# Kernel tuning notes

Measured on AMD Instinct MI355X. Metric: run time of the kernel, lower is better.

## Reference

```python
import jax, jax.numpy as jnp
import numpy as np

N_NODES = 50000
N_EDGES = 800000
F_IN = 16
F_EDGE = 8
H = 8  # latent_dim = [8, 8]
NUM_GRAPHS = 512


def setup_inputs() -> dict:
    key = jax.random.key(0)
    ks = jax.random.split(key, 16)
    x = jax.random.normal(ks[0], (N_NODES, F_IN), dtype=jnp.float32)
    edge_index = jax.random.randint(ks[1], (2, N_EDGES), 0, N_NODES)
    edge_attr = jax.random.normal(ks[2], (N_EDGES, F_EDGE), dtype=jnp.float32)
    batch = jnp.sort(jax.random.randint(ks[3], (N_NODES,), 0, NUM_GRAPHS))
    s = 0.1
    # edge MLPs (single Linear each): edge_attr -> flattened [in, out] weight
    We1 = jax.random.normal(ks[4], (F_EDGE, F_IN * H), dtype=jnp.float32) * s
    be1 = jnp.zeros((F_IN * H,), dtype=jnp.float32)
    We2 = jax.random.normal(ks[5], (F_EDGE, H * H), dtype=jnp.float32) * s
    be2 = jnp.zeros((H * H,), dtype=jnp.float32)
    # NNConv root weights + biases
    root1 = jax.random.normal(ks[6], (F_IN, H), dtype=jnp.float32) * s
    b1 = jnp.zeros((H,), dtype=jnp.float32)
    root2 = jax.random.normal(ks[7], (H, H), dtype=jnp.float32) * s
    b2 = jnp.zeros((H,), dtype=jnp.float32)
    # final readout linear H -> 1
    Wlast = jax.random.normal(ks[8], (H, 1), dtype=jnp.float32) * s
    blast = jnp.zeros((1,), dtype=jnp.float32)
    return {"x": x, "edge_index": edge_index, "edge_attr": edge_attr, "batch": batch,
            "We1": We1, "be1": be1, "root1": root1, "b1": b1,
            "We2": We2, "be2": be2, "root2": root2, "b2": b2,
            "Wlast": Wlast, "blast": blast}


def _nnconv(x, src, dst, edge_attr, We, be, root, b, in_dim, out_dim):
    # per-edge weight matrix from edge MLP: [E, in_dim, out_dim]
    W = (edge_attr @ We + be).reshape(-1, in_dim, out_dim)
    # gather source features, per-edge matvec, scatter-add to targets
    msg = jnp.einsum('ei,eio->eo', x[src], W)            # [E, out_dim]
    agg = jax.ops.segment_sum(msg, dst, num_segments=x.shape[0])
    return agg + x @ root + b                            # root weight + bias


def reference(x, edge_index, edge_attr, batch, We1, be1, root1, b1,
              We2, be2, root2, b2, Wlast, blast):
    src, dst = edge_index[0], edge_index[1]
    h = jax.nn.relu(_nnconv(x, src, dst, edge_attr, We1, be1, root1, b1, F_IN, H))
    h = jax.nn.relu(_nnconv(h, src, dst, edge_attr, We2, be2, root2, b2, H, H))
    # per-graph sum pooling (vectorized equivalent of the python loop)
    pooled = jax.ops.segment_sum(h, batch, num_segments=NUM_GRAPHS)  # [G, H]
    return pooled @ Wlast + blast                                    # [G, 1]
```

## Files before the change

kernel.cpp:

```cpp
#include <hip/hip_runtime.h>

#define F_EDGE 8
#define H 8

__device__ __forceinline__ unsigned short f2bf(float f) {
    unsigned u = __float_as_uint(f);
    unsigned r = u + 0x7fffu + ((u >> 16) & 1u);
    return (unsigned short)(r >> 16);
}
__device__ __forceinline__ float bflo(unsigned u) { return __uint_as_float(u << 16); }
__device__ __forceinline__ float bfhi(unsigned u) { return __uint_as_float(u & 0xffff0000u); }

__global__ __launch_bounds__(256) void pack_kernel(
    const int* __restrict__ ei, const float* __restrict__ ea,
    int2* __restrict__ sd, unsigned short* __restrict__ eab, int E) {
    int e = blockIdx.x * 256 + threadIdx.x;
    if (e >= E) return;
    sd[e] = make_int2(ei[e], ei[E + e]);
    const float4* av = (const float4*)(ea + (long long)e * F_EDGE);
    float4 a0 = av[0], a1 = av[1];
    uint4 pw;
    pw.x = (unsigned)f2bf(a0.x) | ((unsigned)f2bf(a0.y) << 16);
    pw.y = (unsigned)f2bf(a0.z) | ((unsigned)f2bf(a0.w) << 16);
    pw.z = (unsigned)f2bf(a1.x) | ((unsigned)f2bf(a1.y) << 16);
    pw.w = (unsigned)f2bf(a1.z) | ((unsigned)f2bf(a1.w) << 16);
    *(uint4*)(eab + (long long)e * F_EDGE) = pw;
}

template <int IN, bool RELU, bool INIT>
__global__ __launch_bounds__(256) void prep_kernel(
    const float* __restrict__ feat, const float* __restrict__ We,
    const float* __restrict__ be, const float* __restrict__ root,
    const float* __restrict__ b, unsigned short* __restrict__ Pt,
    float* __restrict__ q, float* __restrict__ aggseed, int n_nodes,
    float* __restrict__ out, const float* __restrict__ blast, int out_n) {
    __shared__ float sW[IN * H * 12];
    int tid = threadIdx.x;
    for (int t = tid; t < IN * H * 12; t += 256) {
        int r = t / 12, m = t - r * 12;
        float v = 0.f;
        if (m < 8) v = We[m * (IN * H) + r];
        else if (m == 8) v = be[r];
        else if (m == 9) v = root[r];
        sW[t] = v;
    }
    if (INIT && blockIdx.x == 0) {
        float bl = blast[0];
        for (int t = tid; t < out_n; t += 256) out[t] = bl;
    }
    __syncthreads();

    int n = blockIdx.x * 32 + (tid >> 3);
    if (n >= n_nodes) return;
    int j = tid & 7;

    float f[IN];
    const float4* fv = (const float4*)(feat + (long long)n * IN);
#pragma unroll
    for (int i4 = 0; i4 < IN / 4; ++i4) {
        float4 v = fv[i4];
        f[i4 * 4 + 0] = v.x; f[i4 * 4 + 1] = v.y;
        f[i4 * 4 + 2] = v.z; f[i4 * 4 + 3] = v.w;
    }
    if (RELU) {
#pragma unroll
        for (int i = 0; i < IN; ++i) f[i] = f[i] > 0.f ? f[i] : 0.f;
    }

    float p[8] = {0.f, 0.f, 0.f, 0.f, 0.f, 0.f, 0.f, 0.f};
    float qq = 0.f, hr = 0.f;
#pragma unroll
    for (int i = 0; i < IN; ++i) {
        const float* row = &sW[(i * 8 + j) * 12];
        float4 w0 = *(const float4*)row;
        float4 w1 = *(const float4*)(row + 4);
        float2 br = *(const float2*)(row + 8);
        float fi = f[i];
        p[0] = fmaf(fi, w0.x, p[0]); p[1] = fmaf(fi, w0.y, p[1]);
        p[2] = fmaf(fi, w0.z, p[2]); p[3] = fmaf(fi, w0.w, p[3]);
        p[4] = fmaf(fi, w1.x, p[4]); p[5] = fmaf(fi, w1.y, p[5]);
        p[6] = fmaf(fi, w1.z, p[6]); p[7] = fmaf(fi, w1.w, p[7]);
        qq = fmaf(fi, br.x, qq);
        hr = fmaf(fi, br.y, hr);
    }
    uint4 pw;
    pw.x = (unsigned)f2bf(p[0]) | ((unsigned)f2bf(p[1]) << 16);
    pw.y = (unsigned)f2bf(p[2]) | ((unsigned)f2bf(p[3]) << 16);
    pw.z = (unsigned)f2bf(p[4]) | ((unsigned)f2bf(p[5]) << 16);
    pw.w = (unsigned)f2bf(p[6]) | ((unsigned)f2bf(p[7]) << 16);
    *(uint4*)(Pt + ((long long)n * H + j) * F_EDGE) = pw;
    q[(long long)n * H + j] = qq;
    aggseed[(long long)n * H + j] = hr + b[j];
}

__global__ __launch_bounds__(256) void edge_fact_kernel(
    const int2* __restrict__ sd, const unsigned short* __restrict__ eab,
    const unsigned short* __restrict__ Pt, const float* __restrict__ q,
    float* __restrict__ agg, int E) {
    long long gid = (long long)blockIdx.x * 256 + threadIdx.x;
    int e = (int)(gid >> 3);
    if (e >= E) return;
    int j = (int)(gid & 7);

    int2 se = sd[e];
    uint4 av = *(const uint4*)(eab + (long long)e * F_EDGE);
    uint4 pw = *(const uint4*)(Pt + ((long long)se.x * H + j) * F_EDGE);
    float m = q[(long long)se.x * H + j];

    m = fmaf(bflo(av.x), bflo(pw.x), m);
    m = fmaf(bfhi(av.x), bfhi(pw.x), m);
    m = fmaf(bflo(av.y), bflo(pw.y), m);
    m = fmaf(bfhi(av.y), bfhi(pw.y), m);
    m = fmaf(bflo(av.z), bflo(pw.z), m);
    m = fmaf(bfhi(av.z), bfhi(pw.z), m);
    m = fmaf(bflo(av.w), bflo(pw.w), m);
    m = fmaf(bfhi(av.w), bfhi(pw.w), m);

    unsafeAtomicAdd(&agg[(long long)se.y * H + j], m);
}

__global__ __launch_bounds__(256) void pool_kernel(
    const float* __restrict__ h2pre, const int* __restrict__ batch,
    const float* __restrict__ Wlast, float* __restrict__ out,
    int n_nodes, int n_graphs) {
    __shared__ float bins[512];
    bool use_bins = (n_graphs <= 512);
    if (use_bins) {
        for (int t = threadIdx.x; t < n_graphs; t += 256) bins[t] = 0.f;
        __syncthreads();
    }
    float wl[8];
#pragma unroll
    for (int j = 0; j < 8; ++j) wl[j] = Wlast[j];

    int base = blockIdx.x * 1024;
#pragma unroll
    for (int r = 0; r < 4; ++r) {
        int n = base + r * 256 + threadIdx.x;
        if (n < n_nodes) {
            const float4* hv = (const float4*)(h2pre + (long long)n * H);
            float4 h0 = hv[0], h1 = hv[1];
            float c = 0.f;
            c = fmaf(fmaxf(h0.x, 0.f), wl[0], c);
            c = fmaf(fmaxf(h0.y, 0.f), wl[1], c);
            c = fmaf(fmaxf(h0.z, 0.f), wl[2], c);
            c = fmaf(fmaxf(h0.w, 0.f), wl[3], c);
            c = fmaf(fmaxf(h1.x, 0.f), wl[4], c);
            c = fmaf(fmaxf(h1.y, 0.f), wl[5], c);
            c = fmaf(fmaxf(h1.z, 0.f), wl[6], c);
            c = fmaf(fmaxf(h1.w, 0.f), wl[7], c);
            if (use_bins) atomicAdd(&bins[batch[n]], c);
            else unsafeAtomicAdd(&out[batch[n]], c);
        }
    }
    if (use_bins) {
        __syncthreads();
        for (int t = threadIdx.x; t < n_graphs; t += 256) {
            float v = bins[t];
            if (v != 0.f) unsafeAtomicAdd(&out[t], v);
        }
    }
}

extern "C" void kernel_launch(void* const* d_in, const int* in_sizes, int n_in,
                              void* d_out, int out_size, void* d_ws, size_t ws_size,
                              hipStream_t stream) {
    const float* x     = (const float*)d_in[0];
    const int*   ei    = (const int*)d_in[1];
    const float* ea    = (const float*)d_in[2];
    const int*   batch = (const int*)d_in[3];
    const float* We1   = (const float*)d_in[4];
    const float* be1   = (const float*)d_in[5];
    const float* root1 = (const float*)d_in[6];
    const float* b1    = (const float*)d_in[7];
    const float* We2   = (const float*)d_in[8];
    const float* be2   = (const float*)d_in[9];
    const float* root2 = (const float*)d_in[10];
    const float* b2    = (const float*)d_in[11];
    const float* Wlast = (const float*)d_in[12];
    const float* blast = (const float*)d_in[13];
    float* out = (float*)d_out;

    int F_IN_rt = 16;
    int n_nodes = in_sizes[0] / F_IN_rt;
    int E = in_sizes[1] / 2;

    char* w = (char*)d_ws;
    auto take = [&](size_t bytes) {
        char* p = w;
        w += (bytes + 15) & ~(size_t)15;
        return p;
    };
    unsigned short* Pt1 = (unsigned short*)take((size_t)n_nodes * H * F_EDGE * 2);
    unsigned short* Pt2 = (unsigned short*)take((size_t)n_nodes * H * F_EDGE * 2);
    float* q1    = (float*)take((size_t)n_nodes * H * 4);
    float* q2    = (float*)take((size_t)n_nodes * H * 4);
    float* h1    = (float*)take((size_t)n_nodes * H * 4);
    float* h2    = (float*)take((size_t)n_nodes * H * 4);
    int2* sd     = (int2*)take((size_t)E * 8);
    unsigned short* eab = (unsigned short*)take((size_t)E * F_EDGE * 2);

    int nbe = (E + 255) / 256;

    pack_kernel<<<nbe, 256, 0, stream>>>(ei, ea, sd, eab, E);

    int nblocks = (n_nodes + 31) / 32;
    prep_kernel<16, false, true><<<nblocks, 256, 0, stream>>>(
        x, We1, be1, root1, b1, Pt1, q1, h1, n_nodes, out, blast, out_size);

    long long lanes = (long long)E * H;
    int eblks = (int)((lanes + 255) / 256);
    edge_fact_kernel<<<eblks, 256, 0, stream>>>(sd, eab, Pt1, q1, h1, E);

    prep_kernel<H, true, false><<<nblocks, 256, 0, stream>>>(
        h1, We2, be2, root2, b2, Pt2, q2, h2, n_nodes, nullptr, nullptr, 0);

    edge_fact_kernel<<<eblks, 256, 0, stream>>>(sd, eab, Pt2, q2, h2, E);

    int pblocks = (n_nodes + 1023) / 1024;
    pool_kernel<<<pblocks, 256, 0, stream>>>(h2, batch, Wlast, out, n_nodes, out_size);
}
```

Measured before the change: 204.3 us.

## Fuse all phases into one cooperative persistent kernel with grid syncs

Replaces the six separate launches with one cooperative mega-kernel that runs prep, edge, prep, edge and pool phases, separated by grid-wide barriers and using grid-stride loops. The pack kernel is removed, so edges read the int indices and fp32 edge attributes directly instead of a packed bf16 copy. This aims to cut launch gaps and the extra pass over the edges. In exchange the edge phase reads more bytes per edge, occupancy is capped at a persistent grid, and four grid syncs are added. The old multi-launch path is kept as a fallback if the cooperative launch fails.

Measured after the change: 459.7 us. +125.0%, slower.

```diff
diff --git a/kernel.cpp b/kernel.cpp
--- a/kernel.cpp
+++ b/kernel.cpp
@@ -1,4 +1,7 @@
 #include <hip/hip_runtime.h>
+#include <hip/hip_cooperative_groups.h>
+
+namespace cg = cooperative_groups;
 
 #define F_EDGE 8
 #define H 8
@@ -11,30 +14,14 @@
 __device__ __forceinline__ float bflo(unsigned u) { return __uint_as_float(u << 16); }
 __device__ __forceinline__ float bfhi(unsigned u) { return __uint_as_float(u & 0xffff0000u); }
 
-__global__ __launch_bounds__(256) void pack_kernel(
-    const int* __restrict__ ei, const float* __restrict__ ea,
-    int2* __restrict__ sd, unsigned short* __restrict__ eab, int E) {
-    int e = blockIdx.x * 256 + threadIdx.x;
-    if (e >= E) return;
-    sd[e] = make_int2(ei[e], ei[E + e]);
-    const float4* av = (const float4*)(ea + (long long)e * F_EDGE);
-    float4 a0 = av[0], a1 = av[1];
-    uint4 pw;
-    pw.x = (unsigned)f2bf(a0.x) | ((unsigned)f2bf(a0.y) << 16);
-    pw.y = (unsigned)f2bf(a0.z) | ((unsigned)f2bf(a0.w) << 16);
-    pw.z = (unsigned)f2bf(a1.x) | ((unsigned)f2bf(a1.y) << 16);
-    pw.w = (unsigned)f2bf(a1.z) | ((unsigned)f2bf(a1.w) << 16);
-    *(uint4*)(eab + (long long)e * F_EDGE) = pw;
-}
-
-template <int IN, bool RELU, bool INIT>
-__global__ __launch_bounds__(256) void prep_kernel(
+
+template <int IN, bool RELU>
+__device__ __forceinline__ void prep_phase(
     const float* __restrict__ feat, const float* __restrict__ We,
     const float* __restrict__ be, const float* __restrict__ root,
     const float* __restrict__ b, unsigned short* __restrict__ Pt,
     float* __restrict__ q, float* __restrict__ aggseed, int n_nodes,
-    float* __restrict__ out, const float* __restrict__ blast, int out_n) {
-    __shared__ float sW[IN * H * 12];
+    float* smem) {
     int tid = threadIdx.x;
     for (int t = tid; t < IN * H * 12; t += 256) {
         int r = t / 12, m = t - r * 12;
@@ -42,124 +29,192 @@
         if (m < 8) v = We[m * (IN * H) + r];
         else if (m == 8) v = be[r];
         else if (m == 9) v = root[r];
-        sW[t] = v;
-    }
+        smem[t] = v;
+    }
+    __syncthreads();
+
+    int U = (n_nodes + 31) >> 5;
+    int j = tid & 7;
+    for (int u = blockIdx.x; u < U; u += gridDim.x) {
+        int n = u * 32 + (tid >> 3);
+        if (n >= n_nodes) continue;
+
+        float f[IN];
+        const float4* fv = (const float4*)(feat + (long long)n * IN);
+#pragma unroll
+        for (int i4 = 0; i4 < IN / 4; ++i4) {
+            float4 v = fv[i4];
+            f[i4 * 4 + 0] = v.x; f[i4 * 4 + 1] = v.y;
+            f[i4 * 4 + 2] = v.z; f[i4 * 4 + 3] = v.w;
+        }
+        if (RELU) {
+#pragma unroll
+            for (int i = 0; i < IN; ++i) f[i] = f[i] > 0.f ? f[i] : 0.f;
+        }
+
+        float p[8] = {0.f, 0.f, 0.f, 0.f, 0.f, 0.f, 0.f, 0.f};
+        float qq = 0.f, hr = 0.f;
+#pragma unroll
+        for (int i = 0; i < IN; ++i) {
+            const float* row = &smem[(i * 8 + j) * 12];
+            float4 w0 = *(const float4*)row;
+            float4 w1 = *(const float4*)(row + 4);
+            float2 br = *(const float2*)(row + 8);
+            float fi = f[i];
+            p[0] = fmaf(fi, w0.x, p[0]); p[1] = fmaf(fi, w0.y, p[1]);
+            p[2] = fmaf(fi, w0.z, p[2]); p[3] = fmaf(fi, w0.w, p[3]);
+            p[4] = fmaf(fi, w1.x, p[4]); p[5] = fmaf(fi, w1.y, p[5]);
+            p[6] = fmaf(fi, w1.z, p[6]); p[7] = fmaf(fi, w1.w, p[7]);
+            qq = fmaf(fi, br.x, qq);
+            hr = fmaf(fi, br.y, hr);
+        }
+        uint4 pw;
+        pw.x = (unsigned)f2bf(p[0]) | ((unsigned)f2bf(p[1]) << 16);
+        pw.y = (unsigned)f2bf(p[2]) | ((unsigned)f2bf(p[3]) << 16);
+        pw.z = (unsigned)f2bf(p[4]) | ((unsigned)f2bf(p[5]) << 16);
+        pw.w = (unsigned)f2bf(p[6]) | ((unsigned)f2bf(p[7]) << 16);
+        *(uint4*)(Pt + ((long long)n * H + j) * F_EDGE) = pw;
+        q[(long long)n * H + j] = qq;
+        aggseed[(long long)n * H + j] = hr + b[j];
+    }
+}
+
+__device__ __forceinline__ void edge_phase(
+    const int* __restrict__ ei, const float* __restrict__ ea,
+    const unsigned short* __restrict__ Pt, const float* __restrict__ q,
+    float* __restrict__ agg, int E) {
+    long long total = (long long)E * 8;
+    long long stride = (long long)gridDim.x * 256;
+    for (long long gid = (long long)blockIdx.x * 256 + threadIdx.x;
+         gid < total; gid += stride) {
+        int e = (int)(gid >> 3);
+        int j = (int)(gid & 7);
+
+        int src = ei[e];
+        int dst = ei[E + e];
+
+        const float4* av = (const float4*)(ea + (long long)e * F_EDGE);
+        float4 a0 = av[0], a1 = av[1];
+        uint4 pw = *(const uint4*)(Pt + ((long long)src * H + j) * F_EDGE);
+        float m = q[(long long)src * H + j];
+
+        m = fmaf(a0.x, bflo(pw.x), m);
+        m = fmaf(a0.y, bfhi(pw.x), m);
+        m = fmaf(a0.z, bflo(pw.y), m);
+        m = fmaf(a0.w, bfhi(pw.y), m);
+        m = fmaf(a1.x, bflo(pw.z), m);
+        m = fmaf(a1.y, bfhi(pw.z), m);
+        m = fmaf(a1.z, bflo(pw.w), m);
+        m = fmaf(a1.w, bfhi(pw.w), m);
+
+        unsafeAtomicAdd(&agg[(long long)dst * H + j], m);
+    }
+}
+
+__device__ __forceinline__ void pool_phase(
+    const float* __restrict__ h2pre, const int* __restrict__ batch,
+    const float* __restrict__ Wlast, float* __restrict__ out,
+    int n_nodes, int n_graphs, float* bins) {
+    float wl[8];
+#pragma unroll
+    for (int j = 0; j < 8; ++j) wl[j] = Wlast[j];
+    bool use_bins = (n_graphs <= 512);
+
+    int U = (n_nodes + 1023) >> 10;
+    for (int u = blockIdx.x; u < U; u += gridDim.x) {
+        if (use_bins) {
+            for (int t = threadIdx.x; t < n_graphs; t += 256) bins[t] = 0.f;
+            __syncthreads();
+        }
+        int base = u * 1024;
+#pragma unroll
+        for (int r = 0; r < 4; ++r) {
+            int n = base + r * 256 + threadIdx.x;
+            if (n < n_nodes) {
+                const float4* hv = (const float4*)(h2pre + (long long)n * H);
+                float4 h0 = hv[0], h1 = hv[1];
+                float c = 0.f;
+                c = fmaf(fmaxf(h0.x, 0.f), wl[0], c);
+                c = fmaf(fmaxf(h0.y, 0.f), wl[1], c);
+                c = fmaf(fmaxf(h0.z, 0.f), wl[2], c);
+                c = fmaf(fmaxf(h0.w, 0.f), wl[3], c);
+                c = fmaf(fmaxf(h1.x, 0.f), wl[4], c);
+                c = fmaf(fmaxf(h1.y, 0.f), wl[5], c);
+                c = fmaf(fmaxf(h1.z, 0.f), wl[6], c);
+                c = fmaf(fmaxf(h1.w, 0.f), wl[7], c);
+                if (use_bins) atomicAdd(&bins[batch[n]], c);
+                else unsafeAtomicAdd(&out[batch[n]], c);
+            }
+        }
+        if (use_bins) {
+            __syncthreads();
+            for (int t = threadIdx.x; t < n_graphs; t += 256) {
+                float v = bins[t];
+                if (v != 0.f) unsafeAtomicAdd(&out[t], v);
+            }
+            __syncthreads();
+        }
+    }
+}
+
+
+struct MegaArgs {
+    const float* x; const int* ei; const float* ea; const int* batch;
+    const float* We1; const float* be1; const float* root1; const float* b1;
+    const float* We2; const float* be2; const float* root2; const float* b2;
+    const float* Wlast; const float* blast;
+    float* out;
+    unsigned short* Pt1; unsigned short* Pt2;
+    float* q1; float* q2; float* h1; float* h2;
+    int n_nodes; int E; int out_n;
+};
+
+__global__ __launch_bounds__(256, 4) void mega_kernel(MegaArgs a) {
+    cg::grid_group grid = cg::this_grid();
+    __shared__ float smem[16 * H * 12];
+
+    if (blockIdx.x == 0) {
+        float bl = a.blast[0];
+        for (int t = threadIdx.x; t < a.out_n; t += 256) a.out[t] = bl;
+    }
+    prep_phase<16, false>(a.x, a.We1, a.be1, a.root1, a.b1,
+                          a.Pt1, a.q1, a.h1, a.n_nodes, smem);
+    grid.sync();
+    edge_phase(a.ei, a.ea, a.Pt1, a.q1, a.h1, a.E);
+    grid.sync();
+    prep_phase<H, true>(a.h1, a.We2, a.be2, a.root2, a.b2,
+                        a.Pt2, a.q2, a.h2, a.n_nodes, smem);
+    grid.sync();
+    edge_phase(a.ei, a.ea, a.Pt2, a.q2, a.h2, a.E);
+    grid.sync();
+    pool_phase(a.h2, a.batch, a.Wlast, a.out, a.n_nodes, a.out_n, smem);
+}
+
+
+template <int IN, bool RELU, bool INIT>
+__global__ __launch_bounds__(256) void prep_kernel(
+    const float* feat, const float* We, const float* be, const float* root,
+    const float* b, unsigned short* Pt, float* q, float* aggseed, int n_nodes,
+    float* out, const float* blast, int out_n) {
+    __shared__ float smem[IN * H * 12];
     if (INIT && blockIdx.x == 0) {
         float bl = blast[0];
-        for (int t = tid; t < out_n; t += 256) out[t] = bl;
-    }
-    __syncthreads();
-
-    int n = blockIdx.x * 32 + (tid >> 3);
-    if (n >= n_nodes) return;
-    int j = tid & 7;
-
-    float f[IN];
-    const float4* fv = (const float4*)(feat + (long long)n * IN);
-#pragma unroll
-    for (int i4 = 0; i4 < IN / 4; ++i4) {
-        float4 v = fv[i4];
-        f[i4 * 4 + 0] = v.x; f[i4 * 4 + 1] = v.y;
-        f[i4 * 4 + 2] = v.z; f[i4 * 4 + 3] = v.w;
-    }
-    if (RELU) {
-#pragma unroll
-        for (int i = 0; i < IN; ++i) f[i] = f[i] > 0.f ? f[i] : 0.f;
-    }
-
-    float p[8] = {0.f, 0.f, 0.f, 0.f, 0.f, 0.f, 0.f, 0.f};
-    float qq = 0.f, hr = 0.f;
-#pragma unroll
-    for (int i = 0; i < IN; ++i) {
-        const float* row = &sW[(i * 8 + j) * 12];
-        float4 w0 = *(const float4*)row;
-        float4 w1 = *(const float4*)(row + 4);
-        float2 br = *(const float2*)(row + 8);
-        float fi = f[i];
-        p[0] = fmaf(fi, w0.x, p[0]); p[1] = fmaf(fi, w0.y, p[1]);
-        p[2] = fmaf(fi, w0.z, p[2]); p[3] = fmaf(fi, w0.w, p[3]);
-        p[4] = fmaf(fi, w1.x, p[4]); p[5] = fmaf(fi, w1.y, p[5]);
-        p[6] = fmaf(fi, w1.z, p[6]); p[7] = fmaf(fi, w1.w, p[7]);
-        qq = fmaf(fi, br.x, qq);
-        hr = fmaf(fi, br.y, hr);
-    }
-    uint4 pw;
-    pw.x = (unsigned)f2bf(p[0]) | ((unsigned)f2bf(p[1]) << 16);
-    pw.y = (unsigned)f2bf(p[2]) | ((unsigned)f2bf(p[3]) << 16);
-    pw.z = (unsigned)f2bf(p[4]) | ((unsigned)f2bf(p[5]) << 16);
-    pw.w = (unsigned)f2bf(p[6]) | ((unsigned)f2bf(p[7]) << 16);
-    *(uint4*)(Pt + ((long long)n * H + j) * F_EDGE) = pw;
-    q[(long long)n * H + j] = qq;
-    aggseed[(long long)n * H + j] = hr + b[j];
-}
-
-__global__ __launch_bounds__(256) void edge_fact_kernel(
-    const int2* __restrict__ sd, const unsigned short* __restrict__ eab,
-    const unsigned short* __restrict__ Pt, const float* __restrict__ q,
-    float* __restrict__ agg, int E) {
-    long long gid = (long long)blockIdx.x * 256 + threadIdx.x;
-    int e = (int)(gid >> 3);
-    if (e >= E) return;
-    int j = (int)(gid & 7);
-
-    int2 se = sd[e];
-    uint4 av = *(const uint4*)(eab + (long long)e * F_EDGE);
-    uint4 pw = *(const uint4*)(Pt + ((long long)se.x * H + j) * F_EDGE);
-    float m = q[(long long)se.x * H + j];
-
-    m = fmaf(bflo(av.x), bflo(pw.x), m);
-    m = fmaf(bfhi(av.x), bfhi(pw.x), m);
-    m = fmaf(bflo(av.y), bflo(pw.y), m);
-    m = fmaf(bfhi(av.y), bfhi(pw.y), m);
-    m = fmaf(bflo(av.z), bflo(pw.z), m);
-    m = fmaf(bfhi(av.z), bfhi(pw.z), m);
-    m = fmaf(bflo(av.w), bflo(pw.w), m);
-    m = fmaf(bfhi(av.w), bfhi(pw.w), m);
-
-    unsafeAtomicAdd(&agg[(long long)se.y * H + j], m);
+        for (int t = threadIdx.x; t < out_n; t += 256) out[t] = bl;
+    }
+    prep_phase<IN, RELU>(feat, We, be, root, b, Pt, q, aggseed, n_nodes, smem);
+}
+
+__global__ __launch_bounds__(256) void edge_kernel(
+    const int* ei, const float* ea, const unsigned short* Pt, const float* q,
+    float* agg, int E) {
+    edge_phase(ei, ea, Pt, q, agg, E);
 }
 
 __global__ __launch_bounds__(256) void pool_kernel(
-    const float* __restrict__ h2pre, const int* __restrict__ batch,
-    const float* __restrict__ Wlast, float* __restrict__ out,
+    const float* h2pre, const int* batch, const float* Wlast, float* out,
     int n_nodes, int n_graphs) {
     __shared__ float bins[512];
-    bool use_bins = (n_graphs <= 512);
-    if (use_bins) {
-        for (int t = threadIdx.x; t < n_graphs; t += 256) bins[t] = 0.f;
-        __syncthreads();
-    }
-    float wl[8];
-#pragma unroll
-    for (int j = 0; j < 8; ++j) wl[j] = Wlast[j];
-
-    int base = blockIdx.x * 1024;
-#pragma unroll
-    for (int r = 0; r < 4; ++r) {
-        int n = base + r * 256 + threadIdx.x;
-        if (n < n_nodes) {
-            const float4* hv = (const float4*)(h2pre + (long long)n * H);
-            float4 h0 = hv[0], h1 = hv[1];
-            float c = 0.f;
-            c = fmaf(fmaxf(h0.x, 0.f), wl[0], c);
-            c = fmaf(fmaxf(h0.y, 0.f), wl[1], c);
-            c = fmaf(fmaxf(h0.z, 0.f), wl[2], c);
-            c = fmaf(fmaxf(h0.w, 0.f), wl[3], c);
-            c = fmaf(fmaxf(h1.x, 0.f), wl[4], c);
-            c = fmaf(fmaxf(h1.y, 0.f), wl[5], c);
-            c = fmaf(fmaxf(h1.z, 0.f), wl[6], c);
-            c = fmaf(fmaxf(h1.w, 0.f), wl[7], c);
-            if (use_bins) atomicAdd(&bins[batch[n]], c);
-            else unsafeAtomicAdd(&out[batch[n]], c);
-        }
-    }
-    if (use_bins) {
-        __syncthreads();
-        for (int t = threadIdx.x; t < n_graphs; t += 256) {
-            float v = bins[t];
-            if (v != 0.f) unsafeAtomicAdd(&out[t], v);
-        }
-    }
+    pool_phase(h2pre, batch, Wlast, out, n_nodes, n_graphs, bins);
 }
 
 extern "C" void kernel_launch(void* const* d_in, const int* in_sizes, int n_in,
@@ -193,30 +248,57 @@
     };
     unsigned short* Pt1 = (unsigned short*)take((size_t)n_nodes * H * F_EDGE * 2);
     unsigned short* Pt2 = (unsigned short*)take((size_t)n_nodes * H * F_EDGE * 2);
-    float* q1    = (float*)take((size_t)n_nodes * H * 4);
-    float* q2    = (float*)take((size_t)n_nodes * H * 4);
-    float* h1    = (float*)take((size_t)n_nodes * H * 4);
-    float* h2    = (float*)take((size_t)n_nodes * H * 4);
-    int2* sd     = (int2*)take((size_t)E * 8);
-    unsigned short* eab = (unsigned short*)take((size_t)E * F_EDGE * 2);
-
-    int nbe = (E + 255) / 256;
-
-    pack_kernel<<<nbe, 256, 0, stream>>>(ei, ea, sd, eab, E);
-
-    int nblocks = (n_nodes + 31) / 32;
-    prep_kernel<16, false, true><<<nblocks, 256, 0, stream>>>(
-        x, We1, be1, root1, b1, Pt1, q1, h1, n_nodes, out, blast, out_size);
-
-    long long lanes = (long long)E * H;
-    int eblks = (int)((lanes + 255) / 256);
-    edge_fact_kernel<<<eblks, 256, 0, stream>>>(sd, eab, Pt1, q1, h1, E);
-
-    prep_kernel<H, true, false><<<nblocks, 256, 0, stream>>>(
-        h1, We2, be2, root2, b2, Pt2, q2, h2, n_nodes, nullptr, nullptr, 0);
-
-    edge_fact_kernel<<<eblks, 256, 0, stream>>>(sd, eab, Pt2, q2, h2, E);
-
-    int pblocks = (n_nodes + 1023) / 1024;
-    pool_kernel<<<pblocks, 256, 0, stream>>>(h2, batch, Wlast, out, n_nodes, out_size);
-}
+    float* q1 = (float*)take((size_t)n_nodes * H * 4);
+    float* q2 = (float*)take((size_t)n_nodes * H * 4);
+    float* h1 = (float*)take((size_t)n_nodes * H * 4);
+    float* h2 = (float*)take((size_t)n_nodes * H * 4);
+
+    MegaArgs ka;
+    ka.x = x; ka.ei = ei; ka.ea = ea; ka.batch = batch;
+    ka.We1 = We1; ka.be1 = be1; ka.root1 = root1; ka.b1 = b1;
+    ka.We2 = We2; ka.be2 = be2; ka.root2 = root2; ka.b2 = b2;
+    ka.Wlast = Wlast; ka.blast = blast; ka.out = out;
+    ka.Pt1 = Pt1; ka.Pt2 = Pt2; ka.q1 = q1; ka.q2 = q2; ka.h1 = h1; ka.h2 = h2;
+    ka.n_nodes = n_nodes; ka.E = E; ka.out_n = out_size;
+
+    static int coop_grid = 0;
+    static bool coop_ok = true;
+    if (coop_grid == 0) {
+        int bpc = 0;
+        if (hipOccupancyMaxActiveBlocksPerMultiprocessor(&bpc, mega_kernel, 256, 0)
+                != hipSuccess || bpc <= 0) { bpc = 0; coop_ok = false; }
+        int ncu = 256;
+        hipDeviceProp_t prop;
+        int dev = 0;
+        if (hipGetDevice(&dev) == hipSuccess &&
+            hipGetDeviceProperties(&prop, dev) == hipSuccess &&
+            prop.multiProcessorCount > 0)
+            ncu = prop.multiProcessorCount;
+        coop_grid = bpc * ncu;
+        if (coop_grid <= 0) { coop_grid = 1; coop_ok = false; }
+    }
+
+    bool launched = false;
+    if (coop_ok) {
+        void* kp[] = { (void*)&ka };
+        hipError_t err = hipLaunchCooperativeKernel(
+            (const void*)mega_kernel, dim3(coop_grid), dim3(256), kp, 0, stream);
+        launched = (err == hipSuccess);
+        if (!launched) coop_ok = false;
+    }
+
+    if (!launched) {
+        int nblocks = (n_nodes + 31) / 32;
+        prep_kernel<16, false, true><<<nblocks, 256, 0, stream>>>(
+            x, We1, be1, root1, b1, Pt1, q1, h1, n_nodes, out, blast, out_size);
+        long long lanes = (long long)E * 8;
+        int eblks = (int)((lanes + 255) / 256);
+        edge_kernel<<<eblks, 256, 0, stream>>>(ei, ea, Pt1, q1, h1, E);
+        prep_kernel<H, true, false><<<nblocks, 256, 0, stream>>>(
+            h1, We2, be2, root2, b2, Pt2, q2, h2, n_nodes, nullptr, nullptr, 0);
+        edge_kernel<<<eblks, 256, 0, stream>>>(ei, ea, Pt2, q2, h2, E);
+        int pblocks = (n_nodes + 1023) / 1024;
+        pool_kernel<<<pblocks, 256, 0, stream>>>(h2, batch, Wlast, out,
+                                                 n_nodes, out_size);
+    }
+}
```
